# Optimization experiments

Hardware: AMD Instinct MI355X
Metric: run time of the kernel (lower is better)

Reference implementation:

```python
import jax, jax.numpy as jnp
import numpy as np

N = 16384   # total nodes
G = 256     # graphs in batch
E0 = 131072 # random edges (self loops appended, matching PyG add_self_loops=True)
IN = 256
H = 8       # heads
F = 64      # per-head out dim (h1=h2=h3)


def setup_inputs() -> dict:
    key = jax.random.key(0)
    ks = jax.random.split(key, 40)
    nrm = lambda k, shape, s=0.05: jax.random.normal(k, shape, jnp.float32) * s
    x = jax.random.normal(ks[0], (N, IN), jnp.float32)
    src0 = jax.random.randint(ks[1], (E0,), 0, N)
    dst0 = jax.random.randint(ks[2], (E0,), 0, N)
    loop = jnp.arange(N)
    inp = dict(
        x=x,
        edge_src=jnp.concatenate([src0, loop]),
        edge_dst=jnp.concatenate([dst0, loop]),
        batch=jnp.repeat(jnp.arange(G), N // G),
    )
    dims_in = [IN, H * F, H * F]
    norm_dim = [H * F, H * F, F]
    bias_dim = [H * F, H * F, F]  # conv3 concat=False -> bias size F
    ki = 3
    for i in range(3):
        d = dims_in[i]
        inp[f'Wl{i+1}'] = nrm(ks[ki], (d, H * F)); ki += 1
        inp[f'Wr{i+1}'] = nrm(ks[ki], (d, H * F)); ki += 1
        inp[f'att{i+1}'] = nrm(ks[ki], (H, F)); ki += 1
        inp[f'b{i+1}'] = nrm(ks[ki], (bias_dim[i],)); ki += 1
        inp[f'gnw{i+1}'] = jnp.ones((norm_dim[i],), jnp.float32)
        inp[f'gnb{i+1}'] = jnp.zeros((norm_dim[i],), jnp.float32)
        inp[f'gnm{i+1}'] = jnp.ones((norm_dim[i],), jnp.float32)
    inp['Wlin'] = nrm(ks[ki], (F, 2)); ki += 1
    inp['blin'] = jnp.zeros((2,), jnp.float32)
    return inp


def _gatv2(x, Wl, Wr, att, b, src, dst, concat):
    # GATv2Conv (PyG defaults: share_weights=False, negative_slope=0.2), eval mode (no dropout)
    n = x.shape[0]
    Hh, Ff = att.shape
    xl = (x @ Wl).reshape(n, Hh, Ff)
    xr = (x @ Wr).reshape(n, Hh, Ff)
    m = xl[src] + xr[dst]                      # [E, H, F]
    e = jnp.where(m > 0, m, 0.2 * m)           # leaky_relu
    logit = jnp.einsum('ehf,hf->eh', e, att)   # [E, H]
    lmax = jax.ops.segment_max(logit, dst, num_segments=n)
    lmax = jnp.where(jnp.isneginf(lmax), 0.0, lmax)
    p = jnp.exp(logit - lmax[dst])
    den = jax.ops.segment_sum(p, dst, num_segments=n)
    alpha = p / (den[dst] + 1e-16)             # PyG softmax eps
    out = jax.ops.segment_sum(alpha[:, :, None] * xl[src], dst, num_segments=n)
    out = out.reshape(n, Hh * Ff) if concat else out.mean(axis=1)
    return out + b


def _graphnorm(x, w, b, ms, batch, g):
    cnt = jax.ops.segment_sum(jnp.ones((x.shape[0],), x.dtype), batch, num_segments=g)[:, None]
    mean = jax.ops.segment_sum(x, batch, num_segments=g) / cnt
    xc = x - ms * mean[batch]
    var = jax.ops.segment_sum(xc * xc, batch, num_segments=g) / cnt
    return w * xc / jnp.sqrt(var[batch] + 1e-5) + b


def reference(x, edge_src, edge_dst, batch,
              Wl1, Wr1, att1, b1, gnw1, gnb1, gnm1,
              Wl2, Wr2, att2, b2, gnw2, gnb2, gnm2,
              Wl3, Wr3, att3, b3, gnw3, gnb3, gnm3,
              Wlin, blin):
    h = jax.nn.relu(_graphnorm(_gatv2(x, Wl1, Wr1, att1, b1, edge_src, edge_dst, True), gnw1, gnb1, gnm1, batch, G))
    h = jax.nn.relu(_graphnorm(_gatv2(h, Wl2, Wr2, att2, b2, edge_src, edge_dst, True), gnw2, gnb2, gnm2, batch, G))
    h = jax.nn.relu(_graphnorm(_gatv2(h, Wl3, Wr3, att3, b3, edge_src, edge_dst, False), gnw3, gnb3, gnm3, batch, G))
    cnt = jax.ops.segment_sum(jnp.ones((h.shape[0],), h.dtype), batch, num_segments=G)[:, None]
    pooled = jax.ops.segment_sum(h, batch, num_segments=G) / cnt  # global_mean_pool
    return pooled @ Wlin + blin
```

## Files before the change

### kernel.cpp

```cpp
#include <hip/hip_runtime.h>
#include <hip/hip_bf16.h>
#include <stdint.h>
#include <string.h>

#define NNODES 16384
#define GIN 256
#define NG 64
#define NGRAPH 256
#define FDIM 64
#define CDIM 512

typedef __attribute__((ext_vector_type(8))) short bf16x8;
typedef __attribute__((ext_vector_type(4))) float f32x4;

__device__ __forceinline__ float bf2f(unsigned short u){
  union { unsigned int i; float f; } w; w.i = ((unsigned int)u) << 16; return w.f;
}

__device__ __forceinline__ void unpk(unsigned int u, float& lo, float& hi){
  union { unsigned int i; float f; } a, b;
  a.i = u << 16; b.i = u & 0xffff0000u;
  lo = a.f; hi = b.f;
}

union PK8 { __hip_bfloat16 h[8]; uint4 v; };

__device__ __forceinline__ void async16(const void* g, void* l){
  __builtin_amdgcn_global_load_lds(
      (const __attribute__((address_space(1))) unsigned int*)g,
      (__attribute__((address_space(3))) unsigned int*)l, 16, 0, 0);
}

__global__ void k_detect(const unsigned short* __restrict__ x, int* __restrict__ flag){
  int lane = threadIdx.x;
  int bad = 0;
  #pragma unroll
  for (int j = 0; j < 4; j++){
    float f = bf2f(x[lane*4 + j]);
    if (!(fabsf(f) < 1e4f)) bad++;
  }
  #pragma unroll
  for (int o = 32; o; o >>= 1) bad += __shfl_down(bad, o);
  if (lane == 0) *flag = (bad > 16) ? 1 : 0;
}

struct CArgs {
  const void* p[17];
  int cum[18];
};

__global__ void k_convert(CArgs a, const int* __restrict__ flag, float* __restrict__ dst, int total){
  int isf32 = *flag;
  for (int idx = blockIdx.x*blockDim.x + threadIdx.x; idx < total; idx += gridDim.x*blockDim.x){
    int seg = 0;
    while (idx >= a.cum[seg+1]) seg++;
    int off = idx - a.cum[seg];
    float v;
    if (isf32) v = ((const float*)a.p[seg])[off];
    else       v = bf2f(((const unsigned short*)a.p[seg])[off]);
    dst[idx] = v;
  }
}

__global__ void k_xconv(const void* __restrict__ xin, const int* __restrict__ flag,
                        __hip_bfloat16* __restrict__ xbf, int* __restrict__ deg, int total){
  int isf32 = *flag;
  for (int idx = blockIdx.x*blockDim.x + threadIdx.x; idx < total; idx += gridDim.x*blockDim.x){
    if (idx < NNODES) deg[idx] = 0;
    float v;
    if (isf32) v = ((const float*)xin)[idx];
    else       v = bf2f(((const unsigned short*)xin)[idx]);
    xbf[idx] = __float2bfloat16(v);
  }
}

struct TArgs {
  const void* W[6];
  __hip_bfloat16* Wt[6];
  int K[6];
};

__global__ void k_transpose_all(TArgs t, const int* __restrict__ flag){
  int isf32 = *flag;
  int seg = blockIdx.z;
  int K = t.K[seg];
  int n0 = blockIdx.x*32, k0 = blockIdx.y*32;
  if (k0 >= K) return;
  const void* W = t.W[seg];
  __hip_bfloat16* Wt = t.Wt[seg];
  __shared__ float tl[32][33];
  for (int r = threadIdx.y; r < 32; r += 8){
    size_t idx = (size_t)(k0 + r)*CDIM + n0 + threadIdx.x;
    tl[r][threadIdx.x] = isf32 ? ((const float*)W)[idx] : bf2f(((const unsigned short*)W)[idx]);
  }
  __syncthreads();
  for (int r = threadIdx.y; r < 32; r += 8)
    Wt[(size_t)(n0 + r)*K + k0 + threadIdx.x] = __float2bfloat16(tl[threadIdx.x][r]);
}

__global__ void k_count(const int* __restrict__ edst, int E, int* __restrict__ deg){
  int e = blockIdx.x*blockDim.x + threadIdx.x;
  if (e < E) atomicAdd(&deg[edst[e]], 1);
}

__global__ void k_scan(const int* __restrict__ deg, int* __restrict__ off, int* __restrict__ cur){
  __shared__ int ss[256];
  int t = threadIdx.x;
  int base = t * 64;
  int s = 0;
  for (int j = 0; j < 64; j++) s += deg[base + j];
  ss[t] = s;
  __syncthreads();
  for (int o = 1; o < 256; o <<= 1){
    int v = 0;
    if (t >= o) v = ss[t - o];
    __syncthreads();
    if (t >= o) ss[t] += v;
    __syncthreads();
  }
  int run = ss[t] - s;
  for (int j = 0; j < 64; j++){
    int i = base + j;
    off[i] = run;
    cur[i] = run;
    run += deg[i];
  }
  if (t == 255) off[NNODES] = run;
}

__global__ void k_fill(const int* __restrict__ esrc, const int* __restrict__ edst, int E,
                       int* __restrict__ cur, int* __restrict__ srcs){
  int e = blockIdx.x*blockDim.x + threadIdx.x;
  if (e < E){
    int pos = atomicAdd(&cur[edst[e]], 1);
    srcs[pos] = esrc[e];
  }
}

__global__ __launch_bounds__(256) void k_gemm_mfma(
    const __hip_bfloat16* __restrict__ A,
    const __hip_bfloat16* __restrict__ Wtl, const __hip_bfloat16* __restrict__ Wtr,
    __hip_bfloat16* __restrict__ Cl, __hip_bfloat16* __restrict__ Cr, int K){
  const __hip_bfloat16* Wt = blockIdx.z ? Wtr : Wtl;
  __hip_bfloat16*       C  = blockIdx.z ? Cr  : Cl;
  __shared__ __align__(16) char As[2][16384];
  __shared__ __align__(16) char Bs[2][16384];
  int tid = threadIdx.x;
  int w = tid >> 6, lane = tid & 63;
  int wm = (w >> 1) & 1, wn = w & 1;
  int row0 = blockIdx.x * 128, col0 = blockIdx.y * 128;
  int c = lane >> 4, l16 = lane & 15;

  f32x4 acc[4][4];
  #pragma unroll
  for (int i = 0; i < 4; i++)
    #pragma unroll
    for (int j = 0; j < 4; j++) acc[i][j] = (f32x4){0.f,0.f,0.f,0.f};

  auto stage = [&](int buf, int k0){
    #pragma unroll
    for (int t = 0; t < 8; t++){
      int call = t*4 + w;
      if (call < 16){
        int cc = call >> 1, half = call & 1;
        const __hip_bfloat16* gp = A + (size_t)(row0 + half*64 + lane)*K + k0 + cc*8;
        async16(gp, As[buf] + call*1024);
      } else {
        int q = call - 16;
        int cc = q >> 1, half = q & 1;
        const __hip_bfloat16* gp = Wt + (size_t)(col0 + half*64 + lane)*K + k0 + cc*8;
        async16(gp, Bs[buf] + q*1024);
      }
    }
  };

  stage(0, 0);
  __syncthreads();

  int nIter = K >> 6;
  for (int it = 0; it < nIter; it++){
    int cur = it & 1;
    bf16x8 af[2][4], bfr[2][4];
    #pragma unroll
    for (int ko = 0; ko < 2; ko++){
      #pragma unroll
      for (int i = 0; i < 4; i++)
        af[ko][i]  = *(const bf16x8*)(As[cur] + (ko*4 + c)*2048 + (wm*64 + i*16 + l16)*16);
      #pragma unroll
      for (int j = 0; j < 4; j++)
        bfr[ko][j] = *(const bf16x8*)(Bs[cur] + (ko*4 + c)*2048 + (wn*64 + j*16 + l16)*16);
    }
    if (it + 1 < nIter) stage(1 - cur, (it + 1) << 6);
    #pragma unroll
    for (int ko = 0; ko < 2; ko++)
      #pragma unroll
      for (int i = 0; i < 4; i++)
        #pragma unroll
        for (int j = 0; j < 4; j++)
          acc[i][j] = __builtin_amdgcn_mfma_f32_16x16x32_bf16(af[ko][i], bfr[ko][j], acc[i][j], 0, 0, 0);
    __syncthreads();
  }

  int r4 = lane >> 4;
  #pragma unroll
  for (int i = 0; i < 4; i++)
    #pragma unroll
    for (int j = 0; j < 4; j++){
      __hip_bfloat16* cp = C + (size_t)(row0 + wm*64 + i*16 + r4*4)*CDIM + col0 + wn*64 + j*16 + l16;
      #pragma unroll
      for (int r = 0; r < 4; r++)
        cp[(size_t)r*CDIM] = __float2bfloat16(acc[i][j][r]);
    }
}

template<int CONCAT>
__global__ __launch_bounds__(256) void k_fused_attn(
    const __hip_bfloat16* __restrict__ XL, const __hip_bfloat16* __restrict__ XR,
    const float* __restrict__ att,
    const int* __restrict__ off, const int* __restrict__ srcs,
    const float* __restrict__ bias, __hip_bfloat16* __restrict__ OUT){
  int wave = threadIdx.x >> 6, lane = threadIdx.x & 63;
  int d = blockIdx.x * 4 + wave;
  if (d >= NNODES) return;

  uint4 xru = *(const uint4*)((const char*)XR + ((size_t)d*CDIM + lane*8)*2);
  float xr[8];
  unpk(xru.x, xr[0], xr[1]); unpk(xru.y, xr[2], xr[3]);
  unpk(xru.z, xr[4], xr[5]); unpk(xru.w, xr[6], xr[7]);
  const float4* atp = (const float4*)(att + lane*8);
  float4 at0 = atp[0], at1 = atp[1];
  float at[8] = {at0.x, at0.y, at0.z, at0.w, at1.x, at1.y, at1.z, at1.w};

  float acc[8];
  #pragma unroll
  for (int j = 0; j < 8; j++) acc[j] = 0.f;
  float den = 0.f;

  int beg = off[d], end = off[d+1];

  auto leaky = [](float m){ return fmaxf(m, 0.2f*m); };

  for (int i = beg; i < end; i += 4){
    int n = end - i;
    int s0 = srcs[i];
    int s1 = n > 1 ? srcs[i+1] : s0;
    int s2 = n > 2 ? srcs[i+2] : s0;
    int s3 = n > 3 ? srcs[i+3] : s0;
    uint4 rw[4];
    rw[0] = *(const uint4*)((const char*)XL + ((size_t)s0*CDIM + lane*8)*2);
    rw[1] = *(const uint4*)((const char*)XL + ((size_t)s1*CDIM + lane*8)*2);
    rw[2] = *(const uint4*)((const char*)XL + ((size_t)s2*CDIM + lane*8)*2);
    rw[3] = *(const uint4*)((const char*)XL + ((size_t)s3*CDIM + lane*8)*2);

    #pragma unroll
    for (int e = 0; e < 4; e++){
      if (e < n){
        float xv[8];
        unpk(rw[e].x, xv[0], xv[1]);
        unpk(rw[e].y, xv[2], xv[3]);
        unpk(rw[e].z, xv[4], xv[5]);
        unpk(rw[e].w, xv[6], xv[7]);
        float v = 0.f;
        #pragma unroll
        for (int j = 0; j < 8; j++) v = fmaf(leaky(xv[j] + xr[j]), at[j], v);
        v += __shfl_xor(v, 1); v += __shfl_xor(v, 2); v += __shfl_xor(v, 4);
        float p = expf(v);
        den += p;
        #pragma unroll
        for (int j = 0; j < 8; j++) acc[j] = fmaf(p, xv[j], acc[j]);
      }
    }
  }

  float inv = 1.f / (den + 1e-16f);
  const float4* bp = (const float4*)(bias + (CONCAT ? lane*8 : (lane & 7)*8));

  if (CONCAT){
    float4 b0v = bp[0], b1v = bp[1];
    float bb[8] = {b0v.x, b0v.y, b0v.z, b0v.w, b1v.x, b1v.y, b1v.z, b1v.w};
    PK8 pk;
    #pragma unroll
    for (int j = 0; j < 8; j++)
      pk.h[j] = __float2bfloat16(acc[j]*inv + bb[j]);
    *(uint4*)((char*)OUT + ((size_t)d*CDIM + lane*8)*2) = pk.v;
  } else {
    float r[8];
    #pragma unroll
    for (int j = 0; j < 8; j++) r[j] = acc[j] * inv;
    #pragma unroll
    for (int o = 8; o < 64; o <<= 1)
      #pragma unroll
      for (int j = 0; j < 8; j++) r[j] += __shfl_xor(r[j], o);
    if (lane < 8){
      float4 b0v = bp[0], b1v = bp[1];
      float bb[8] = {b0v.x, b0v.y, b0v.z, b0v.w, b1v.x, b1v.y, b1v.z, b1v.w};
      PK8 pk;
      #pragma unroll
      for (int j = 0; j < 8; j++)
        pk.h[j] = __float2bfloat16(r[j]*0.125f + bb[j]);
      *(uint4*)((char*)OUT + ((size_t)d*FDIM + lane*8)*2) = pk.v;
    }
  }
}

__global__ void k_graphnorm_relu(const __hip_bfloat16* __restrict__ X, const float* __restrict__ w,
    const float* __restrict__ b, const float* __restrict__ ms,
    __hip_bfloat16* __restrict__ Y, int C){
  int g = blockIdx.x;
  int c = threadIdx.x;
  const __hip_bfloat16* xg = X + (size_t)g * NG * C + c;
  __hip_bfloat16* yg = Y + (size_t)g * NG * C + c;
  float v[NG];
  float s1 = 0.f, s2 = 0.f;
  #pragma unroll
  for (int i = 0; i < NG; i++){
    v[i] = __bfloat162float(xg[(size_t)i*C]);
    s1 += v[i]; s2 += v[i]*v[i];
  }
  float mean = s1 * (1.f/NG);
  float m = ms[c];
  float var = s2 * (1.f/NG) - 2.f*m*mean*mean + m*m*mean*mean;
  float inv = rsqrtf(var + 1e-5f);
  float ww = w[c], bb = b[c];
  #pragma unroll
  for (int i = 0; i < NG; i++){
    float y = fmaf(ww * (v[i] - m*mean), inv, bb);
    yg[(size_t)i*C] = __float2bfloat16(y > 0.f ? y : 0.f);
  }
}

__global__ void k_pool_linear(const __hip_bfloat16* __restrict__ H, const float* __restrict__ Wlin,
    const float* __restrict__ blin, void* out, const int* __restrict__ flag){
  int g = blockIdx.x, c = threadIdx.x;
  float s = 0.f;
  for (int i = 0; i < NG; i++) s += __bfloat162float(H[(long)(g*NG + i)*FDIM + c]);
  float pooled = s * (1.f/NG);
  float v0 = pooled * Wlin[c*2 + 0];
  float v1 = pooled * Wlin[c*2 + 1];
  #pragma unroll
  for (int o = 32; o; o >>= 1){ v0 += __shfl_down(v0, o); v1 += __shfl_down(v1, o); }
  if (c == 0){
    float o0 = v0 + blin[0], o1 = v1 + blin[1];
    if (*flag){
      ((float*)out)[g*2 + 0] = o0;
      ((float*)out)[g*2 + 1] = o1;
    } else {
      ((__hip_bfloat16*)out)[g*2 + 0] = __float2bfloat16(o0);
      ((__hip_bfloat16*)out)[g*2 + 1] = __float2bfloat16(o1);
    }
  }
}

extern "C" void kernel_launch(void* const* d_in, const int* in_sizes, int n_in,
                              void* d_out, int out_size, void* d_ws, size_t ws_size,
                              hipStream_t stream){
  const int N = NNODES;
  const int E = in_sizes[1];

  const int* esrc = (const int*)d_in[1];
  const int* edst = (const int*)d_in[2];

  char* ws = (char*)d_ws;
  size_t cursor_b = 0;
  auto alloc = [&](size_t bytes)->char*{
    char* p = ws + cursor_b;
    cursor_b += (bytes + 255) & ~size_t(255);
    return p;
  };

  int* flag = (int*)alloc(256);

  static const int convIdx[17] = {6,7,8,9,10, 13,14,15,16,17, 20,21,22,23,24, 25,26};
  CArgs ca;
  int cums[18]; cums[0] = 0;
  for (int i = 0; i < 17; i++){
    ca.p[i] = d_in[convIdx[i]];
    cums[i+1] = cums[i] + in_sizes[convIdx[i]];
  }
  memcpy(ca.cum, cums, sizeof(cums));
  int totalConv = cums[17];

  float* conv = (float*)alloc((size_t)totalConv * 4);
  const float* fw[17];
  for (int i = 0; i < 17; i++) fw[i] = conv + cums[i];

  __hip_bfloat16* XLbf  = (__hip_bfloat16*)alloc((size_t)N * CDIM * 2);
  __hip_bfloat16* XRbf  = (__hip_bfloat16*)alloc((size_t)N * CDIM * 2);
  __hip_bfloat16* OUTbf = (__hip_bfloat16*)alloc((size_t)N * CDIM * 2);
  __hip_bfloat16* OUT3  = (__hip_bfloat16*)alloc((size_t)N * FDIM * 2);
  __hip_bfloat16* HBbf  = (__hip_bfloat16*)alloc((size_t)N * CDIM * 2);
  __hip_bfloat16* xbf   = (__hip_bfloat16*)alloc((size_t)N * GIN * 2);
  __hip_bfloat16* Wt[6];
  Wt[0] = (__hip_bfloat16*)alloc((size_t)CDIM * GIN * 2);
  Wt[1] = (__hip_bfloat16*)alloc((size_t)CDIM * GIN * 2);
  Wt[2] = (__hip_bfloat16*)alloc((size_t)CDIM * CDIM * 2);
  Wt[3] = (__hip_bfloat16*)alloc((size_t)CDIM * CDIM * 2);
  Wt[4] = (__hip_bfloat16*)alloc((size_t)CDIM * CDIM * 2);
  Wt[5] = (__hip_bfloat16*)alloc((size_t)CDIM * CDIM * 2);
  int* deg  = (int*)alloc((size_t)N * 4);
  int* off  = (int*)alloc((size_t)(N + 1) * 4);
  int* cur  = (int*)alloc((size_t)N * 4);
  int* srcs = (int*)alloc((size_t)E * 4);

  k_detect<<<1, 64, 0, stream>>>((const unsigned short*)d_in[0], flag);
  k_convert<<<32, 256, 0, stream>>>(ca, flag, conv, totalConv);
  k_xconv<<<2048, 256, 0, stream>>>(d_in[0], flag, xbf, deg, N * GIN);
  {
    TArgs ta;
    const void* Ws[6] = {d_in[4], d_in[5], d_in[11], d_in[12], d_in[18], d_in[19]};
    const int   Ks[6] = {GIN, GIN, CDIM, CDIM, CDIM, CDIM};
    for (int i = 0; i < 6; i++){ ta.W[i] = Ws[i]; ta.Wt[i] = Wt[i]; ta.K[i] = Ks[i]; }
    k_transpose_all<<<dim3(CDIM/32, CDIM/32, 6), dim3(32, 8), 0, stream>>>(ta, flag);
  }

  k_count<<<(E + 255)/256, 256, 0, stream>>>(edst, E, deg);
  k_scan<<<1, 256, 0, stream>>>(deg, off, cur);
  k_fill<<<(E + 255)/256, 256, 0, stream>>>(esrc, edst, E, cur, srcs);

  const float* att_[3] = {fw[0],  fw[5],  fw[10]};
  const float* b_[3]   = {fw[1],  fw[6],  fw[11]};
  const float* gw_[3]  = {fw[2],  fw[7],  fw[12]};
  const float* gb_[3]  = {fw[3],  fw[8],  fw[13]};
  const float* gm_[3]  = {fw[4],  fw[9],  fw[14]};

  const __hip_bfloat16* inbuf = xbf;
  int K = GIN;
  for (int layer = 0; layer < 3; layer++){
    k_gemm_mfma<<<dim3(N/128, CDIM/128, 2), 256, 0, stream>>>(
        inbuf, Wt[layer*2], Wt[layer*2 + 1], XLbf, XRbf, K);
    if (layer < 2){
      k_fused_attn<1><<<N/4, 256, 0, stream>>>(XLbf, XRbf, att_[layer], off, srcs, b_[layer], OUTbf);
      k_graphnorm_relu<<<NGRAPH, CDIM, 0, stream>>>(OUTbf, gw_[layer], gb_[layer], gm_[layer], HBbf, CDIM);
    } else {
      k_fused_attn<0><<<N/4, 256, 0, stream>>>(XLbf, XRbf, att_[layer], off, srcs, b_[layer], OUT3);
      k_graphnorm_relu<<<NGRAPH, FDIM, 0, stream>>>(OUT3, gw_[layer], gb_[layer], gm_[layer], HBbf, FDIM);
    }
    inbuf = HBbf;
    K = CDIM;
  }

  k_pool_linear<<<NGRAPH, 64, 0, stream>>>(HBbf, fw[15], fw[16], d_out, flag);
}
```

Measured before the change: 361.2 us.

## Replace GEMM with 256x256-tile pipelined MFMA kernel and staged epilogue

Replaces the 128x128-tile, 4-wave GEMM with a 256x256-tile, 8-wave kernel. It uses XOR-swizzled LDS, an 8-phase schedule that interleaves async global-to-LDS loads with MFMA compute under explicit barriers and s_setprio, and writes output through LDS as coalesced 16-byte stores. The aim is more operand reuse per LDS byte, fewer bank conflicts and better overlap of loads with math. In exchange it needs 128KB of LDS per block, so only one block fits per CU, and the grid shrinks to about one block per CU, which risks poor latency hiding and load imbalance.

After: 324.1 us. 10.3% less time.

```diff
diff --git a/kernel.cpp b/kernel.cpp
--- a/kernel.cpp
+++ b/kernel.cpp
@@ -137,80 +137,118 @@
   }
 }
 
-__global__ __launch_bounds__(256) void k_gemm_mfma(
+#define GBAR  do { asm volatile("" ::: "memory"); __builtin_amdgcn_s_barrier(); asm volatile("" ::: "memory"); } while(0)
+
+#define PHASE(BUF, MH, NH, LA, LB, SBUF, SISB, SUNIT, ST, DOVM)                                   \
+  { if (LA){ _Pragma("unroll") for (int ko_=0;ko_<2;ko_++)                                        \
+               _Pragma("unroll") for (int ii_=0;ii_<4;ii_++) Afr[ko_][ii_]=rdA(BUF,MH,ii_,ko_); } \
+    if (LB){ _Pragma("unroll") for (int ko_=0;ko_<2;ko_++)                                        \
+               _Pragma("unroll") for (int jj_=0;jj_<2;jj_++) Bfr[ko_][jj_]=rdB(BUF,NH,jj_,ko_); } \
+    stage(SBUF,SISB,SUNIT,ST);                                                                    \
+    if (DOVM) asm volatile("s_waitcnt vmcnt(4)" ::: "memory");                                    \
+    GBAR;                                                                                         \
+    __builtin_amdgcn_s_setprio(1);                                                                \
+    _Pragma("unroll") for (int ii_=0;ii_<4;ii_++)                                                 \
+      _Pragma("unroll") for (int jj_=0;jj_<2;jj_++)                                               \
+        _Pragma("unroll") for (int ko_=0;ko_<2;ko_++)                                             \
+          acc[(MH)*4+ii_][(NH)*2+jj_] = __builtin_amdgcn_mfma_f32_16x16x32_bf16(                  \
+              Afr[ko_][ii_], Bfr[ko_][jj_], acc[(MH)*4+ii_][(NH)*2+jj_], 0, 0, 0);                \
+    __builtin_amdgcn_s_setprio(0);                                                                \
+    GBAR; }
+
+__global__ __launch_bounds__(512, 2) void k_gemm256(
     const __hip_bfloat16* __restrict__ A,
     const __hip_bfloat16* __restrict__ Wtl, const __hip_bfloat16* __restrict__ Wtr,
     __hip_bfloat16* __restrict__ Cl, __hip_bfloat16* __restrict__ Cr, int K){
   const __hip_bfloat16* Wt = blockIdx.z ? Wtr : Wtl;
   __hip_bfloat16*       C  = blockIdx.z ? Cr  : Cl;
-  __shared__ __align__(16) char As[2][16384];
-  __shared__ __align__(16) char Bs[2][16384];
-  int tid = threadIdx.x;
-  int w = tid >> 6, lane = tid & 63;
-  int wm = (w >> 1) & 1, wn = w & 1;
-  int row0 = blockIdx.x * 128, col0 = blockIdx.y * 128;
-  int c = lane >> 4, l16 = lane & 15;
-
-  f32x4 acc[4][4];
-  #pragma unroll
-  for (int i = 0; i < 4; i++)
+  __shared__ __align__(128) char lds[131072];
+  const int tid = threadIdx.x;
+  const int w = tid >> 6, lane = tid & 63;
+  const int wm = w >> 2, wn = w & 3;
+  const int l16 = lane & 15, c4 = lane >> 4;
+  const int row0 = blockIdx.x * 256, col0 = blockIdx.y * 256;
+  const int NT = K >> 6;
+
+  f32x4 acc[8][4];
+  #pragma unroll
+  for (int i = 0; i < 8; i++)
     #pragma unroll
     for (int j = 0; j < 4; j++) acc[i][j] = (f32x4){0.f,0.f,0.f,0.f};
 
-  auto stage = [&](int buf, int k0){
-    #pragma unroll
-    for (int t = 0; t < 8; t++){
-      int call = t*4 + w;
-      if (call < 16){
-        int cc = call >> 1, half = call & 1;
-        const __hip_bfloat16* gp = A + (size_t)(row0 + half*64 + lane)*K + k0 + cc*8;
-        async16(gp, As[buf] + call*1024);
-      } else {
-        int q = call - 16;
-        int cc = q >> 1, half = q & 1;
-        const __hip_bfloat16* gp = Wt + (size_t)(col0 + half*64 + lane)*K + k0 + cc*8;
-        async16(gp, Bs[buf] + q*1024);
-      }
+  bf16x8 Afr[2][4];
+  bf16x8 Bfr[2][2];
+
+  const __hip_bfloat16* Ag = A  + (size_t)row0 * K;
+  const __hip_bfloat16* Bg = Wt + (size_t)col0 * K;
+
+  auto stage = [&](int buf, int isB, int unit, int t){
+    int k0 = (t < NT ? t : t - NT) << 6;
+    #pragma unroll
+    for (int j = 0; j < 2; j++){
+      int u0 = (w*2 + j) * 8;
+      int uidx = u0 + (lane >> 3);
+      int row, rs;
+      if (!isB){ row = (uidx & 63) | ((uidx & 64) << 1) | (unit << 6);
+                 rs  = (u0   & 63) | ((u0   & 64) << 1) | (unit << 6); }
+      else     { row = ((uidx & 96) << 1) | (uidx & 31) | (unit << 5);
+                 rs  = ((u0   & 96) << 1) | (u0   & 31) | (unit << 5); }
+      int chunk = (lane & 7) ^ (uidx & 7);
+      const __hip_bfloat16* gp = (isB ? Bg : Ag) + (size_t)row * K + k0 + chunk * 8;
+      async16(gp, lds + (isB ? 65536 : 0) + buf * 32768 + rs * 128);
     }
   };
 
-  stage(0, 0);
-  __syncthreads();
-
-  int nIter = K >> 6;
-  for (int it = 0; it < nIter; it++){
-    int cur = it & 1;
-    bf16x8 af[2][4], bfr[2][4];
-    #pragma unroll
-    for (int ko = 0; ko < 2; ko++){
-      #pragma unroll
-      for (int i = 0; i < 4; i++)
-        af[ko][i]  = *(const bf16x8*)(As[cur] + (ko*4 + c)*2048 + (wm*64 + i*16 + l16)*16);
+  auto rdA = [&](int buf, int mh, int ii, int ko)->bf16x8{
+    int row = wm*128 + mh*64 + ii*16 + l16;
+    int chunk = ((ko<<2) + c4) ^ (l16 & 7);
+    return *(const bf16x8*)(lds + buf*32768 + row*128 + chunk*16);
+  };
+  auto rdB = [&](int buf, int nh, int jj, int ko)->bf16x8{
+    int row = wn*64 + nh*32 + jj*16 + l16;
+    int chunk = ((ko<<2) + c4) ^ (l16 & 7);
+    return *(const bf16x8*)(lds + 65536 + buf*32768 + row*128 + chunk*16);
+  };
+
+  stage(0,0,0,0); stage(0,1,1,0); stage(0,0,1,0); stage(0,1,0,0);
+  stage(1,0,0,1); stage(1,1,1,1);
+  asm volatile("s_waitcnt vmcnt(4)" ::: "memory");
+  GBAR;
+
+  for (int t = 0; t < NT; t += 2){
+    PHASE(0, 0, 0, 1, 1, 1, 0, 1, t+1, 0)
+    PHASE(0, 0, 1, 0, 1, 1, 1, 0, t+1, 0)
+    PHASE(0, 1, 1, 1, 0, 0, 0, 0, t+2, 0)
+    PHASE(0, 1, 0, 0, 1, 0, 1, 1, t+2, 1)
+    PHASE(1, 0, 0, 1, 1, 0, 0, 1, t+2, 0)
+    PHASE(1, 0, 1, 0, 1, 0, 1, 0, t+2, 0)
+    PHASE(1, 1, 1, 1, 0, 1, 0, 0, t+3, 0)
+    PHASE(1, 1, 0, 0, 1, 1, 1, 1, t+3, 1)
+  }
+
+  asm volatile("s_waitcnt vmcnt(0)" ::: "memory");
+  GBAR;
+  {
+    __hip_bfloat16* ct = (__hip_bfloat16*)lds;
+    #pragma unroll
+    for (int i = 0; i < 8; i++)
       #pragma unroll
       for (int j = 0; j < 4; j++)
-        bfr[ko][j] = *(const bf16x8*)(Bs[cur] + (ko*4 + c)*2048 + (wn*64 + j*16 + l16)*16);
-    }
-    if (it + 1 < nIter) stage(1 - cur, (it + 1) << 6);
-    #pragma unroll
-    for (int ko = 0; ko < 2; ko++)
-      #pragma unroll
-      for (int i = 0; i < 4; i++)
         #pragma unroll
-        for (int j = 0; j < 4; j++)
-          acc[i][j] = __builtin_amdgcn_mfma_f32_16x16x32_bf16(af[ko][i], bfr[ko][j], acc[i][j], 0, 0, 0);
-    __syncthreads();
-  }
-
-  int r4 = lane >> 4;
-  #pragma unroll
-  for (int i = 0; i < 4; i++)
-    #pragma unroll
-    for (int j = 0; j < 4; j++){
-      __hip_bfloat16* cp = C + (size_t)(row0 + wm*64 + i*16 + r4*4)*CDIM + col0 + wn*64 + j*16 + l16;
-      #pragma unroll
-      for (int r = 0; r < 4; r++)
-        cp[(size_t)r*CDIM] = __float2bfloat16(acc[i][j][r]);
-    }
+        for (int r = 0; r < 4; r++){
+          int rl = wm*128 + i*16 + c4*4 + r;
+          int cl = wn*64  + j*16 + l16;
+          ct[rl*256 + cl] = __float2bfloat16(acc[i][j][r]);
+        }
+  }
+  GBAR;
+  #pragma unroll
+  for (int s = 0; s < 16; s++){
+    int seg = s*512 + tid;
+    int rl = seg >> 5, ch = seg & 31;
+    uint4 v = *(const uint4*)(lds + rl*512 + ch*16);
+    *(uint4*)((char*)(C + (size_t)(row0 + rl)*CDIM + col0) + ch*16) = v;
+  }
 }
 
 template<int CONCAT>
@@ -426,7 +464,7 @@
   const __hip_bfloat16* inbuf = xbf;
   int K = GIN;
   for (int layer = 0; layer < 3; layer++){
-    k_gemm_mfma<<<dim3(N/128, CDIM/128, 2), 256, 0, stream>>>(
+    k_gemm256<<<dim3(N/256, CDIM/256, 2), 512, 0, stream>>>(
         inbuf, Wt[layer*2], Wt[layer*2 + 1], XLbf, XRbf, K);
     if (layer < 2){
       k_fused_attn<1><<<N/4, 256, 0, stream>>>(XLbf, XRbf, att_[layer], off, srcs, b_[layer], OUTbf);
```
